# Optimization experiments

Hardware: AMD Instinct MI355X
Metric: run time of the kernel (lower is better)

Reference implementation:

```python
import jax, jax.numpy as jnp
import numpy as np
from jax.ops import segment_sum, segment_max

N_NODES = 100000
N_EDGES = 1600000
IN, HID, OUT = 256, 64, 40
NEG_SLOPE = 0.2  # DGL GATConv default


def setup_inputs() -> dict:
    key = jax.random.key(0)
    ks = jax.random.split(key, 12)
    feat = jax.random.normal(ks[0], (N_NODES, IN), dtype=jnp.float32)
    src = jax.random.randint(ks[1], (N_EDGES,), 0, N_NODES)
    dst = jax.random.randint(ks[2], (N_EDGES,), 0, N_NODES)
    def xavier(k, shape):
        fan = sum(shape)
        return jax.random.normal(k, shape, dtype=jnp.float32) * jnp.sqrt(2.0 / fan)
    return {
        "feat": feat, "src": src, "dst": dst,
        "W1": xavier(ks[3], (IN, HID)),  "b1": jnp.zeros((HID,), jnp.float32),
        "al1": xavier(ks[4], (HID,)),    "ar1": xavier(ks[5], (HID,)),
        "W2": xavier(ks[6], (HID, OUT)), "b2": jnp.zeros((OUT,), jnp.float32),
        "al2": xavier(ks[7], (OUT,)),    "ar2": xavier(ks[8], (OUT,)),
    }


def gat_layer(x, W, b, attn_l, attn_r, src, dst, n):
    # z: [N, F_out] projected features
    z = x @ W
    el = z @ attn_l          # [N] source attention logits
    er = z @ attn_r          # [N] destination attention logits
    e = jax.nn.leaky_relu(el[src] + er[dst], NEG_SLOPE)  # [E]
    # segment (per-destination) softmax over incoming edges
    m = segment_max(e, dst, num_segments=n)              # [N]
    w = jnp.exp(e - m[dst])                              # [E]
    s = segment_sum(w, dst, num_segments=n)              # [N]
    alpha = w / s[dst]                                   # [E]
    # scatter-add aggregation of alpha * z[src]
    out = segment_sum(alpha[:, None] * z[src], dst, num_segments=n)
    return out + b


def reference(feat, src, dst, W1, b1, al1, ar1, W2, b2, al2, ar2):
    n = feat.shape[0]
    h = gat_layer(feat, W1, b1, al1, ar1, src, dst, n)
    h = jax.nn.relu(h)  # dropout is identity in eval mode
    h = gat_layer(h, W2, b2, al2, ar2, src, dst, n)
    return jax.nn.log_softmax(h, axis=-1)  # [N, out_size]
```

## Files before the change

kernel.cpp:

```cpp
#include <hip/hip_runtime.h>
#include <math.h>

constexpr int NN   = 100000;
constexpr int NE   = 1600000;
constexpr int FIN  = 256;
constexpr int HID  = 64;
constexpr int FOUT = 40;
constexpr float SLOPE = 0.2f;
constexpr int NB    = (NN + 255) / 256;
constexpr int NBUCK = NB;
constexpr int TILE_A = 8192;
constexpr int NWG_A = (NE + TILE_A - 1) / TILE_A;
constexpr int AK = 264;

typedef short  short8  __attribute__((ext_vector_type(8)));
typedef float  floatx4 __attribute__((ext_vector_type(4)));

__device__ inline unsigned short f2bf(float x) {
    union { float f; unsigned int u; } c; c.f = x;
    unsigned int u = c.u;
    return (unsigned short)((u + 0x7FFF + ((u >> 16) & 1)) >> 16);
}

__global__ __launch_bounds__(256) void w1t_kernel(
    const float* __restrict__ W1, unsigned short* __restrict__ W1T)
{
    int idx = blockIdx.x * 256 + threadIdx.x;
    if (idx < FIN * HID) {
        int k = idx >> 6, n = idx & 63;
        W1T[n * FIN + k] = f2bf(W1[idx]);
    }
}

__global__ __launch_bounds__(256) void gemm1_kernel(
    const float* __restrict__ feat, const unsigned short* __restrict__ W1T,
    const float* __restrict__ al, const float* __restrict__ ar,
    const int* __restrict__ dst, int* __restrict__ deg,
    float* __restrict__ z, float* __restrict__ el, float* __restrict__ er)
{
    {
        int base = (blockIdx.x * 256 + threadIdx.x) * 4;
        if (base < NE) {
            const int4 d4 = *(const int4*)&dst[base];
            atomicAdd(&deg[d4.x], 1); atomicAdd(&deg[d4.y], 1);
            atomicAdd(&deg[d4.z], 1); atomicAdd(&deg[d4.w], 1);
        }
    }

    __shared__ unsigned short sA[64 * AK];
    __shared__ unsigned short sBT[64 * AK];
    const int t = threadIdx.x;
    const int ntile = blockIdx.x * 64;

    #pragma unroll
    for (int i = 0; i < 16; ++i) {
        int g = t + 256 * i;
        int row = g >> 6, kq = g & 63;
        int n = ntile + row; if (n >= NN) n = NN - 1;
        float4 f = *(const float4*)&feat[(size_t)n * FIN + 4 * kq];
        ushort4 us; us.x = f2bf(f.x); us.y = f2bf(f.y); us.z = f2bf(f.z); us.w = f2bf(f.w);
        *(ushort4*)&sA[row * AK + 4 * kq] = us;
    }
    #pragma unroll
    for (int i = 0; i < 8; ++i) {
        int g = t + 256 * i;
        int row = g >> 5, c8 = g & 31;
        *(uint4*)&sBT[row * AK + 8 * c8] = *(const uint4*)&W1T[row * FIN + 8 * c8];
    }
    __syncthreads();

    const int w  = t >> 6;
    const int l  = t & 63;
    const int lr = l & 15;
    const int q  = l >> 4;
    const int m0 = 16 * w;

    floatx4 acc[4];
    #pragma unroll
    for (int tile = 0; tile < 4; ++tile) acc[tile] = 0.f;

    #pragma unroll
    for (int kc = 0; kc < 8; ++kc) {
        const int koff = kc * 32 + 8 * q;
        const short8 av = *(const short8*)(sA + (m0 + lr) * AK + koff);
        #pragma unroll
        for (int tile = 0; tile < 4; ++tile) {
            const short8 bv = *(const short8*)(sBT + (16 * tile + lr) * AK + koff);
            acc[tile] = __builtin_amdgcn_mfma_f32_16x16x32_bf16(av, bv, acc[tile], 0, 0, 0);
        }
    }

    float aln[4], arn[4];
    #pragma unroll
    for (int tile = 0; tile < 4; ++tile) {
        aln[tile] = al[16 * tile + lr];
        arn[tile] = ar[16 * tile + lr];
    }
    #pragma unroll
    for (int r = 0; r < 4; ++r) {
        int mg = ntile + m0 + 4 * q + r;
        float pl = 0.f, pr = 0.f;
        #pragma unroll
        for (int tile = 0; tile < 4; ++tile) {
            float zv = acc[tile][r];
            pl += zv * aln[tile]; pr += zv * arn[tile];
        }
        #pragma unroll
        for (int off = 8; off >= 1; off >>= 1) {
            pl += __shfl_xor(pl, off);
            pr += __shfl_xor(pr, off);
        }
        if (mg < NN) {
            #pragma unroll
            for (int tile = 0; tile < 4; ++tile)
                z[(size_t)mg * HID + 16 * tile + lr] = acc[tile][r];
            if (lr == 0) { el[mg] = pl; er[mg] = pr; }
        }
    }
}

__global__ __launch_bounds__(256) void gemm2_kernel(
    const float* __restrict__ h, const float* __restrict__ W2,
    const float* __restrict__ al, const float* __restrict__ ar,
    float* __restrict__ z2, float* __restrict__ el, float* __restrict__ er)
{
    __shared__ float sh[4][64];
    const int w = threadIdx.x >> 6, lane = threadIdx.x & 63;
    const int n = blockIdx.x * 4 + w;
    sh[w][lane] = h[(size_t)n * HID + lane];
    __syncthreads();
    float acc = 0.f;
    if (lane < FOUT) {
        #pragma unroll 8
        for (int k = 0; k < 64; ++k) acc += sh[w][k] * W2[k * FOUT + lane];
    }
    float pl = (lane < FOUT) ? acc * al[lane] : 0.f;
    float pr = (lane < FOUT) ? acc * ar[lane] : 0.f;
    #pragma unroll
    for (int off = 32; off >= 1; off >>= 1) { pl += __shfl_xor(pl, off); pr += __shfl_xor(pr, off); }
    if (lane == 0) { el[n] = pl; er[n] = pr; }
    if (lane < FOUT) z2[(size_t)n * FOUT + lane] = acc;
}

__global__ __launch_bounds__(256) void scan_reduce_kernel(
    const int* __restrict__ deg, int* __restrict__ bsum)
{
    __shared__ int tmp[256];
    int idx = blockIdx.x * 256 + threadIdx.x;
    int v = (idx < NN) ? deg[idx] : 0;
    tmp[threadIdx.x] = v; __syncthreads();
    for (int off = 128; off >= 1; off >>= 1) {
        if (threadIdx.x < off) tmp[threadIdx.x] += tmp[threadIdx.x + off];
        __syncthreads();
    }
    if (threadIdx.x == 0) bsum[blockIdx.x] = tmp[0];
}

__global__ __launch_bounds__(512) void scan_top_kernel(
    const int* __restrict__ bsum, int* __restrict__ bofs, int* __restrict__ row_ptr)
{
    __shared__ int tmp[512];
    int t = threadIdx.x;
    int v = (t < NB) ? bsum[t] : 0;
    tmp[t] = v; __syncthreads();
    for (int off = 1; off < 512; off <<= 1) {
        int x = (t >= off) ? tmp[t - off] : 0;
        __syncthreads();
        tmp[t] += x;
        __syncthreads();
    }
    int excl = tmp[t] - v;
    if (t < NB) bofs[t] = excl;
    if (t == NB - 1) row_ptr[NN] = excl + v;
}

__global__ __launch_bounds__(256) void scan_final_kernel(
    const int* __restrict__ deg, const int* __restrict__ bofs,
    int* __restrict__ row_ptr, int* __restrict__ gcur)
{
    __shared__ int tmp[256];
    int t = threadIdx.x;
    int idx = blockIdx.x * 256 + t;
    int v = (idx < NN) ? deg[idx] : 0;
    tmp[t] = v; __syncthreads();
    for (int off = 1; off < 256; off <<= 1) {
        int x = (t >= off) ? tmp[t - off] : 0;
        __syncthreads();
        tmp[t] += x;
        __syncthreads();
    }
    if (idx < NN) row_ptr[idx] = bofs[blockIdx.x] + tmp[t] - v;
    if (t == 0) gcur[blockIdx.x] = bofs[blockIdx.x];
}

__global__ __launch_bounds__(256) void partitionA_kernel(
    const int* __restrict__ src, const int* __restrict__ dst,
    int* __restrict__ gcur, int* __restrict__ ebuck)
{
    __shared__ int hist[NBUCK];
    __shared__ int lcur[NBUCK];
    const int t = threadIdx.x;
    const int e0 = blockIdx.x * TILE_A;
    const int e1 = (e0 + TILE_A < NE) ? e0 + TILE_A : NE;

    for (int i = t; i < NBUCK; i += 256) hist[i] = 0;
    __syncthreads();
    for (int e = e0 + t; e < e1; e += 256)
        atomicAdd(&hist[dst[e] >> 8], 1);
    __syncthreads();
    for (int i = t; i < NBUCK; i += 256) {
        int hv = hist[i];
        lcur[i] = hv ? atomicAdd(&gcur[i], hv) : 0;
    }
    __syncthreads();
    for (int e = e0 + t; e < e1; e += 256) {
        int d = dst[e], s = src[e];
        int p = atomicAdd(&lcur[d >> 8], 1);
        ebuck[p] = (s << 8) | (d & 255);
    }
}

__global__ __launch_bounds__(256) void partitionB_kernel(
    const int* __restrict__ row_ptr, const int* __restrict__ ebuck,
    int* __restrict__ esrc)
{
    __shared__ int lcur[256];
    const int b = blockIdx.x;
    const int n0 = b << 8;
    const int n1 = (n0 + 256 < NN) ? n0 + 256 : NN;
    const int t = threadIdx.x;
    if (n0 + t < n1) lcur[t] = row_ptr[n0 + t];
    __syncthreads();
    const int r0 = row_ptr[n0], r1 = row_ptr[n1];
    for (int e = r0 + t; e < r1; e += 256) {
        int pk = ebuck[e];
        int p = atomicAdd(&lcur[pk & 255], 1);
        esrc[p] = pk >> 8;
    }
}

template<int F, bool FINAL_LAYER>
__global__ __launch_bounds__(256) void gat_gather_kernel(
    const int* __restrict__ row_ptr, const int* __restrict__ esrc,
    const float* __restrict__ el, const float* __restrict__ er,
    const float* __restrict__ z, const float* __restrict__ bias,
    float* __restrict__ out)
{
    __shared__ float sw[4][64];
    __shared__ int   ssn[4][64];
    const int w = threadIdx.x >> 6, lane = threadIdx.x & 63;
    const int d = blockIdx.x * 4 + w;
    const int r0 = row_ptr[d], r1 = row_ptr[d + 1];
    const int cnt = r1 - r0;
    const float erd = er[d];

    float accv = 0.f;
    float s = 0.f;

    if (cnt <= 64) {
        int sn = 0; float v = -INFINITY;
        if (lane < cnt) {
            sn = esrc[r0 + lane];
            v = el[sn] + erd;
            v = (v >= 0.f) ? v : SLOPE * v;
        }
        float m = v;
        #pragma unroll
        for (int off = 32; off >= 1; off >>= 1) m = fmaxf(m, __shfl_xor(m, off));
        float wv = (lane < cnt) ? __expf(v - m) : 0.f;
        s = wv;
        #pragma unroll
        for (int off = 32; off >= 1; off >>= 1) s += __shfl_xor(s, off);
        sw[w][lane] = wv; ssn[w][lane] = sn;
        if (lane < F) {
            int j = 0;
            for (; j + 8 <= cnt; j += 8) {
                float acc0 = 0.f, acc1 = 0.f;
                #pragma unroll
                for (int qq = 0; qq < 8; qq += 2) {
                    float wa = sw[w][j + qq],     wb = sw[w][j + qq + 1];
                    int   sa = ssn[w][j + qq],    sb = ssn[w][j + qq + 1];
                    acc0 += wa * z[(size_t)sa * F + lane];
                    acc1 += wb * z[(size_t)sb * F + lane];
                }
                accv += acc0 + acc1;
            }
            for (; j < cnt; ++j)
                accv += sw[w][j] * z[(size_t)ssn[w][j] * F + lane];
        }
    } else {
        float m = -INFINITY;
        for (int e = r0 + lane; e < r1; e += 64) {
            float v = el[esrc[e]] + erd;
            v = (v >= 0.f) ? v : SLOPE * v;
            m = fmaxf(m, v);
        }
        #pragma unroll
        for (int off = 32; off >= 1; off >>= 1) m = fmaxf(m, __shfl_xor(m, off));
        for (int base = r0; base < r1; base += 64) {
            int e = base + lane;
            float wv = 0.f; int sn = 0;
            if (e < r1) {
                sn = esrc[e];
                float v = el[sn] + erd;
                v = (v >= 0.f) ? v : SLOPE * v;
                wv = __expf(v - m);
            }
            sw[w][lane] = wv; ssn[w][lane] = sn;
            s += wv;
            int c = r1 - base; if (c > 64) c = 64;
            if (lane < F) {
                for (int j = 0; j < c; ++j)
                    accv += sw[w][j] * z[(size_t)ssn[w][j] * F + lane];
            }
        }
        #pragma unroll
        for (int off = 32; off >= 1; off >>= 1) s += __shfl_xor(s, off);
    }

    float res = (cnt > 0) ? (accv / s) : 0.f;

    if (!FINAL_LAYER) {
        if (lane < F) {
            float v = res + bias[lane];
            out[(size_t)d * F + lane] = (v > 0.f) ? v : 0.f;
        }
    } else {
        float v = (lane < F) ? res + bias[lane] : -INFINITY;
        float mx = v;
        #pragma unroll
        for (int off = 32; off >= 1; off >>= 1) mx = fmaxf(mx, __shfl_xor(mx, off));
        float ex = (lane < F) ? __expf(v - mx) : 0.f;
        float sm = ex;
        #pragma unroll
        for (int off = 32; off >= 1; off >>= 1) sm += __shfl_xor(sm, off);
        if (lane < F) out[(size_t)d * F + lane] = v - mx - __logf(sm);
    }
}

extern "C" void kernel_launch(void* const* d_in, const int* in_sizes, int n_in,
                              void* d_out, int out_size, void* d_ws, size_t ws_size,
                              hipStream_t stream) {
    const float* feat = (const float*)d_in[0];
    const int*   src  = (const int*)d_in[1];
    const int*   dst  = (const int*)d_in[2];
    const float* W1   = (const float*)d_in[3];
    const float* b1   = (const float*)d_in[4];
    const float* al1  = (const float*)d_in[5];
    const float* ar1  = (const float*)d_in[6];
    const float* W2   = (const float*)d_in[7];
    const float* b2   = (const float*)d_in[8];
    const float* al2  = (const float*)d_in[9];
    const float* ar2  = (const float*)d_in[10];
    float* out = (float*)d_out;

    float* ws    = (float*)d_ws;
    float* z1    = ws;
    float* h     = z1 + (size_t)NN * HID;
    float* el1   = h + (size_t)NN * HID;
    float* er1   = el1 + NN;
    float* el2   = er1 + NN;
    float* er2   = el2 + NN;
    int*   deg   = (int*)(er2 + NN);
    int*   rowp  = deg + NN;
    int*   bsum  = rowp + NN + 1;
    int*   bofs  = bsum + NB;
    int*   gcur  = bofs + NB;
    int*   esrc  = gcur + NBUCK;
    unsigned short* w1t = (unsigned short*)(esrc + NE);
    int*   ebuck = (int*)h;
    float* z2    = z1;

    hipMemsetAsync(deg, 0, NN * sizeof(int), stream);

    w1t_kernel<<<(FIN * HID + 255) / 256, 256, 0, stream>>>(W1, w1t);
    gemm1_kernel<<<(NN + 63) / 64, 256, 0, stream>>>(feat, w1t, al1, ar1, dst, deg, z1, el1, er1);

    scan_reduce_kernel<<<NB, 256, 0, stream>>>(deg, bsum);
    scan_top_kernel<<<1, 512, 0, stream>>>(bsum, bofs, rowp);
    scan_final_kernel<<<NB, 256, 0, stream>>>(deg, bofs, rowp, gcur);
    partitionA_kernel<<<NWG_A, 256, 0, stream>>>(src, dst, gcur, ebuck);
    partitionB_kernel<<<NBUCK, 256, 0, stream>>>(rowp, ebuck, esrc);

    gat_gather_kernel<HID, false><<<NN / 4, 256, 0, stream>>>(rowp, esrc, el1, er1, z1, b1, h);

    gemm2_kernel<<<NN / 4, 256, 0, stream>>>(h, W2, al2, ar2, z2, el2, er2);
    gat_gather_kernel<FOUT, true><<<NN / 4, 256, 0, stream>>>(rowp, esrc, el2, er2, z2, b2, out);
}
```

Measured before the change: 468.6 us.

## Replace per-node degree atomics with bucket histogram and per-bucket local scan

The per-node global degree atomics and the two-level global scan are replaced by a per-block shared-memory histogram of 256-node buckets, flushed to a small global bucket count array. partitionB then derives per-node degrees and row_ptr with a local scan inside each bucket. This removes two scan kernels and about 1.6M global atomics. Separately, gemm1 now reads feat rows straight from global memory into MFMA A fragments and converts them to bf16 in registers, skipping the shared-memory A tile. In exchange, the A loads are less coalesced, and partitionB reads each bucket's edges twice.

```diff
diff --git a/kernel.cpp b/kernel.cpp
--- a/kernel.cpp
+++ b/kernel.cpp
@@ -35,32 +35,15 @@
 __global__ __launch_bounds__(256) void gemm1_kernel(
     const float* __restrict__ feat, const unsigned short* __restrict__ W1T,
     const float* __restrict__ al, const float* __restrict__ ar,
-    const int* __restrict__ dst, int* __restrict__ deg,
+    const int* __restrict__ dst, int* __restrict__ bcnt,
     float* __restrict__ z, float* __restrict__ el, float* __restrict__ er)
 {
-    {
-        int base = (blockIdx.x * 256 + threadIdx.x) * 4;
-        if (base < NE) {
-            const int4 d4 = *(const int4*)&dst[base];
-            atomicAdd(&deg[d4.x], 1); atomicAdd(&deg[d4.y], 1);
-            atomicAdd(&deg[d4.z], 1); atomicAdd(&deg[d4.w], 1);
-        }
-    }
-
-    __shared__ unsigned short sA[64 * AK];
     __shared__ unsigned short sBT[64 * AK];
+    __shared__ int hist[NBUCK];
     const int t = threadIdx.x;
     const int ntile = blockIdx.x * 64;
 
-    #pragma unroll
-    for (int i = 0; i < 16; ++i) {
-        int g = t + 256 * i;
-        int row = g >> 6, kq = g & 63;
-        int n = ntile + row; if (n >= NN) n = NN - 1;
-        float4 f = *(const float4*)&feat[(size_t)n * FIN + 4 * kq];
-        ushort4 us; us.x = f2bf(f.x); us.y = f2bf(f.y); us.z = f2bf(f.z); us.w = f2bf(f.w);
-        *(ushort4*)&sA[row * AK + 4 * kq] = us;
-    }
+    for (int i = t; i < NBUCK; i += 256) hist[i] = 0;
     #pragma unroll
     for (int i = 0; i < 8; ++i) {
         int g = t + 256 * i;
@@ -68,6 +51,20 @@
         *(uint4*)&sBT[row * AK + 8 * c8] = *(const uint4*)&W1T[row * FIN + 8 * c8];
     }
     __syncthreads();
+
+    {
+        int base = (blockIdx.x * 256 + t) * 4;
+        if (base < NE) {
+            const int4 d4 = *(const int4*)&dst[base];
+            atomicAdd(&hist[d4.x >> 8], 1); atomicAdd(&hist[d4.y >> 8], 1);
+            atomicAdd(&hist[d4.z >> 8], 1); atomicAdd(&hist[d4.w >> 8], 1);
+        }
+    }
+    __syncthreads();
+    for (int i = t; i < NBUCK; i += 256) {
+        int hv = hist[i];
+        if (hv) atomicAdd(&bcnt[i], hv);
+    }
 
     const int w  = t >> 6;
     const int l  = t & 63;
@@ -75,6 +72,9 @@
     const int q  = l >> 4;
     const int m0 = 16 * w;
 
+    int n = ntile + m0 + lr; if (n >= NN) n = NN - 1;
+    const float* __restrict__ arow = feat + (size_t)n * FIN;
+
     floatx4 acc[4];
     #pragma unroll
     for (int tile = 0; tile < 4; ++tile) acc[tile] = 0.f;
@@ -82,7 +82,13 @@
     #pragma unroll
     for (int kc = 0; kc < 8; ++kc) {
         const int koff = kc * 32 + 8 * q;
-        const short8 av = *(const short8*)(sA + (m0 + lr) * AK + koff);
+        const float4 fa = *(const float4*)(arow + koff);
+        const float4 fb = *(const float4*)(arow + koff + 4);
+        short8 av;
+        av[0] = (short)f2bf(fa.x); av[1] = (short)f2bf(fa.y);
+        av[2] = (short)f2bf(fa.z); av[3] = (short)f2bf(fa.w);
+        av[4] = (short)f2bf(fb.x); av[5] = (short)f2bf(fb.y);
+        av[6] = (short)f2bf(fb.z); av[7] = (short)f2bf(fb.w);
         #pragma unroll
         for (int tile = 0; tile < 4; ++tile) {
             const short8 bv = *(const short8*)(sBT + (16 * tile + lr) * AK + koff);
@@ -142,26 +148,12 @@
     if (lane < FOUT) z2[(size_t)n * FOUT + lane] = acc;
 }
 
-__global__ __launch_bounds__(256) void scan_reduce_kernel(
-    const int* __restrict__ deg, int* __restrict__ bsum)
-{
-    __shared__ int tmp[256];
-    int idx = blockIdx.x * 256 + threadIdx.x;
-    int v = (idx < NN) ? deg[idx] : 0;
-    tmp[threadIdx.x] = v; __syncthreads();
-    for (int off = 128; off >= 1; off >>= 1) {
-        if (threadIdx.x < off) tmp[threadIdx.x] += tmp[threadIdx.x + off];
-        __syncthreads();
-    }
-    if (threadIdx.x == 0) bsum[blockIdx.x] = tmp[0];
-}
-
 __global__ __launch_bounds__(512) void scan_top_kernel(
-    const int* __restrict__ bsum, int* __restrict__ bofs, int* __restrict__ row_ptr)
+    const int* __restrict__ bcnt, int* __restrict__ bofs, int* __restrict__ gcur)
 {
     __shared__ int tmp[512];
     int t = threadIdx.x;
-    int v = (t < NB) ? bsum[t] : 0;
+    int v = (t < NB) ? bcnt[t] : 0;
     tmp[t] = v; __syncthreads();
     for (int off = 1; off < 512; off <<= 1) {
         int x = (t >= off) ? tmp[t - off] : 0;
@@ -170,27 +162,8 @@
         __syncthreads();
     }
     int excl = tmp[t] - v;
-    if (t < NB) bofs[t] = excl;
-    if (t == NB - 1) row_ptr[NN] = excl + v;
-}
-
-__global__ __launch_bounds__(256) void scan_final_kernel(
-    const int* __restrict__ deg, const int* __restrict__ bofs,
-    int* __restrict__ row_ptr, int* __restrict__ gcur)
-{
-    __shared__ int tmp[256];
-    int t = threadIdx.x;
-    int idx = blockIdx.x * 256 + t;
-    int v = (idx < NN) ? deg[idx] : 0;
-    tmp[t] = v; __syncthreads();
-    for (int off = 1; off < 256; off <<= 1) {
-        int x = (t >= off) ? tmp[t - off] : 0;
-        __syncthreads();
-        tmp[t] += x;
-        __syncthreads();
-    }
-    if (idx < NN) row_ptr[idx] = bofs[blockIdx.x] + tmp[t] - v;
-    if (t == 0) gcur[blockIdx.x] = bofs[blockIdx.x];
+    if (t < NB) { bofs[t] = excl; gcur[t] = excl; }
+    if (t == NB - 1) bofs[NB] = excl + v;
 }
 
 __global__ __launch_bounds__(256) void partitionA_kernel(
@@ -221,20 +194,40 @@
 }
 
 __global__ __launch_bounds__(256) void partitionB_kernel(
-    const int* __restrict__ row_ptr, const int* __restrict__ ebuck,
-    int* __restrict__ esrc)
-{
-    __shared__ int lcur[256];
+    const int* __restrict__ bofs, const int* __restrict__ ebuck,
+    int* __restrict__ row_ptr, int* __restrict__ esrc)
+{
+    __shared__ int sdeg[256];
+    __shared__ int sscan[256];
     const int b = blockIdx.x;
     const int n0 = b << 8;
-    const int n1 = (n0 + 256 < NN) ? n0 + 256 : NN;
     const int t = threadIdx.x;
-    if (n0 + t < n1) lcur[t] = row_ptr[n0 + t];
-    __syncthreads();
-    const int r0 = row_ptr[n0], r1 = row_ptr[n1];
+    const int r0 = bofs[b], r1 = bofs[b + 1];
+
+    sdeg[t] = 0;
+    __syncthreads();
+    for (int e = r0 + t; e < r1; e += 256)
+        atomicAdd(&sdeg[ebuck[e] & 255], 1);
+    __syncthreads();
+
+    int v = sdeg[t];
+    sscan[t] = v;
+    __syncthreads();
+    for (int off = 1; off < 256; off <<= 1) {
+        int x = (t >= off) ? sscan[t - off] : 0;
+        __syncthreads();
+        sscan[t] += x;
+        __syncthreads();
+    }
+    int excl = sscan[t] - v;
+    if (n0 + t < NN) row_ptr[n0 + t] = r0 + excl;
+    if (b == NBUCK - 1 && t == 0) row_ptr[NN] = NE;
+
+    sdeg[t] = r0 + excl;
+    __syncthreads();
     for (int e = r0 + t; e < r1; e += 256) {
         int pk = ebuck[e];
-        int p = atomicAdd(&lcur[pk & 255], 1);
+        int p = atomicAdd(&sdeg[pk & 255], 1);
         esrc[p] = pk >> 8;
     }
 }
@@ -361,26 +354,23 @@
     float* er1   = el1 + NN;
     float* el2   = er1 + NN;
     float* er2   = el2 + NN;
-    int*   deg   = (int*)(er2 + NN);
-    int*   rowp  = deg + NN;
-    int*   bsum  = rowp + NN + 1;
-    int*   bofs  = bsum + NB;
-    int*   gcur  = bofs + NB;
-    int*   esrc  = gcur + NBUCK;
+    int*   bcnt  = (int*)(er2 + NN);
+    int*   bofs  = bcnt + NB;
+    int*   gcur  = bofs + NB + 1;
+    int*   rowp  = gcur + NBUCK;
+    int*   esrc  = rowp + NN + 1;
     unsigned short* w1t = (unsigned short*)(esrc + NE);
     int*   ebuck = (int*)h;
     float* z2    = z1;
 
-    hipMemsetAsync(deg, 0, NN * sizeof(int), stream);
+    hipMemsetAsync(bcnt, 0, NB * sizeof(int), stream);
 
     w1t_kernel<<<(FIN * HID + 255) / 256, 256, 0, stream>>>(W1, w1t);
-    gemm1_kernel<<<(NN + 63) / 64, 256, 0, stream>>>(feat, w1t, al1, ar1, dst, deg, z1, el1, er1);
-
-    scan_reduce_kernel<<<NB, 256, 0, stream>>>(deg, bsum);
-    scan_top_kernel<<<1, 512, 0, stream>>>(bsum, bofs, rowp);
-    scan_final_kernel<<<NB, 256, 0, stream>>>(deg, bofs, rowp, gcur);
+    gemm1_kernel<<<(NN + 63) / 64, 256, 0, stream>>>(feat, w1t, al1, ar1, dst, bcnt, z1, el1, er1);
+
+    scan_top_kernel<<<1, 512, 0, stream>>>(bcnt, bofs, gcur);
     partitionA_kernel<<<NWG_A, 256, 0, stream>>>(src, dst, gcur, ebuck);
-    partitionB_kernel<<<NBUCK, 256, 0, stream>>>(rowp, ebuck, esrc);
+    partitionB_kernel<<<NBUCK, 256, 0, stream>>>(bofs, ebuck, rowp, esrc);
 
     gat_gather_kernel<HID, false><<<NN / 4, 256, 0, stream>>>(rowp, esrc, el1, er1, z1, b1, h);
 
```

Result: faster. 441.8 us (-5.7%).
